# Optimization experiments

Measured on AMD Instinct MI355X. Metric: run time of the kernel, lower is better.

## Reference

```python
import jax, jax.numpy as jnp
import numpy as np

NQ = 11          # qubits per atom
NL = 3           # circuit layers (and message-passing layers)
S = 2 ** NQ      # statevector size
PAD = 100        # feature-map input width


def setup_inputs() -> dict:
    key = jax.random.key(0)
    ks = jax.random.split(key, 18)
    B, A, F, E = 8, 96, 64, 384
    return {
        "node_features": jax.random.normal(ks[0], (B, A, F), jnp.float32),
        "edge_indices": jax.random.randint(ks[1], (2, E), 0, A),
        # QuantumFeatureMap.feature_preprocessor: Linear(100,64) -> ReLU -> Linear(64,NQ) -> Tanh
        "W1": jax.random.normal(ks[2], (64, PAD), jnp.float32) * 0.1,
        "b1": jnp.zeros((64,), jnp.float32),
        "W2": jax.random.normal(ks[3], (NQ, 64), jnp.float32) * 0.1,
        "b2": jnp.zeros((NQ,), jnp.float32),
        # QuantumFeatureMap circuit params
        "rot": jax.random.normal(ks[4], (NL, NQ, 3), jnp.float32),
        "ent": jax.random.normal(ks[5], (NL, NQ - 1), jnp.float32),
        # one QuantumMessagePassing layer per NL, each with message_gates [NQ,3]
        "msg_gates": jax.random.normal(ks[6], (NL, NQ, 3), jnp.float32),
        # QuantumGlobalPooling
        "pool_w": jax.random.normal(ks[7], (NQ,), jnp.float32),
        # output MLP: Linear(2*NQ,256)->ReLU->Linear(256,128)->ReLU->Linear(128,64)
        "Wo1": jax.random.normal(ks[8], (256, 2 * NQ), jnp.float32) * 0.1,
        "bo1": jnp.zeros((256,), jnp.float32),
        "Wo2": jax.random.normal(ks[9], (128, 256), jnp.float32) * 0.05,
        "bo2": jnp.zeros((128,), jnp.float32),
        "Wo3": jax.random.normal(ks[10], (64, 128), jnp.float32) * 0.05,
        "bo3": jnp.zeros((64,), jnp.float32),
    }


def _apply_rotation(amps, M, q):
    """Apply per-batch 2x2 gate M [N,2,2] on qubit q of amps [N,S]."""
    N = amps.shape[0]
    lo = 1 << q
    hi = S // (2 * lo)
    a = amps.reshape(N, hi, 2, lo)  # bit q of state index is the middle axis
    return jnp.einsum('nij,nhjl->nhil', M, a).reshape(N, S)


def _forward(node_features, W1, b1, W2, b2, rot, ent, msg_gates, pool_w,
             Wo1, bo1, Wo2, bo2, Wo3, bo3):
    B, A, F = node_features.shape
    N = B * A
    # --- QuantumNodeEmbedding: pad atom features to 100, shared feature map ---
    x = node_features.reshape(N, F)
    x = jnp.pad(x, ((0, 0), (0, PAD - F)))
    h = jax.nn.relu(x @ W1.T + b1)
    f = jnp.tanh(h @ W2.T + b2)            # [N, NQ] per-qubit angles scaling
    amps = jnp.zeros((N, S), jnp.complex64).at[:, 0].set(1.0)
    states = jnp.arange(S)
    # --- QuantumFeatureMap circuit ---
    for l in range(NL):
        for q in range(NQ):
            rx = rot[l, q, 0] * f[:, q]
            ry = rot[l, q, 1] * f[:, q]
            rz = rot[l, q, 2] * f[:, q]
            cx, sx = jnp.cos(rx / 2), jnp.sin(rx / 2)
            cy, sy = jnp.cos(ry / 2), jnp.sin(ry / 2)
            cz, sz = jnp.cos(rz / 2), jnp.sin(rz / 2)
            # rotation matrix exactly as in the torch source
            M = jnp.stack([cx * cy * cz, -sx * sy * sz,
                           sx * sy * cz,  cx * cy * sz], -1)
            M = M.reshape(N, 2, 2).astype(jnp.complex64)
            amps = _apply_rotation(amps, M, q)
        for q in range(NQ - 1):
            # parameterized CNOT: for control-bit==1, mix state with target-flipped partner
            p = jax.nn.sigmoid(ent[l, q]).astype(jnp.complex64)
            ctrl = (states >> q) & 1
            partner = states ^ (1 << (q + 1))
            mixed = (1 - p) * amps + p * amps[:, partner]
            amps = jnp.where(ctrl[None, :] == 1, mixed, amps)
    # --- QuantumMessagePassing layers: diagonal phase exp(i*sum(theta_q over set bits)) ---
    bits = ((states[:, None] >> jnp.arange(NQ)[None, :]) & 1).astype(jnp.float32)  # [S,NQ]
    for l in range(NL):
        theta = msg_gates[l].sum(-1)                 # [NQ] rx+ry+rz per qubit
        phase = jnp.exp(1j * (bits @ theta))         # [S] complex64
        amps = amps * phase[None, :]
    # --- QuantumGlobalPooling ---
    amps_b = amps.reshape(B, A, S)
    w = jax.nn.sigmoid(pool_w[jnp.arange(A) % NQ]).astype(jnp.complex64)  # atom i -> w[i%NQ]
    pooled = jnp.einsum('a,bas->bs', w, amps_b)      # [B,S] complex
    norm = jnp.sqrt(jnp.sum(pooled.real ** 2 + pooled.imag ** 2, axis=1, keepdims=True))
    pooled = pooled / jnp.maximum(norm, 1e-12)
    rm = jnp.tile(pooled.real.mean(1, keepdims=True), (1, NQ))
    im = jnp.tile(pooled.imag.mean(1, keepdims=True), (1, NQ))
    rep = jnp.concatenate([rm, im], axis=1)          # [B, 2*NQ]
    # --- output network ---
    h1 = jax.nn.relu(rep @ Wo1.T + bo1)
    h2 = jax.nn.relu(h1 @ Wo2.T + bo2)
    return h2 @ Wo3.T + bo3                          # [B, 64]


def reference(node_features, edge_indices, W1, b1, W2, b2, rot, ent, msg_gates,
              pool_w, Wo1, bo1, Wo2, bo2, Wo3, bo3):
    # edge_indices is accepted by the torch module but does not enter the math
    del edge_indices
    return _forward(node_features, W1, b1, W2, b2, rot, ent, msg_gates, pool_w,
                    Wo1, bo1, Wo2, bo2, Wo3, bo3)
```

## Files before the change

kernel.cpp:

```cpp
#include <hip/hip_runtime.h>

#define NQ 11
#define NL 3
#define S  2048
#define NB 8
#define NA 96
#define NF 64
#define PADW 100
#define WPB 4
#define PPB (NA / WPB)

__device__ __forceinline__ float sigmoidf_(float x) { return 1.0f / (1.0f + expf(-x)); }

__global__ __launch_bounds__(256) void circuit_kernel(
    const float* __restrict__ nf,
    const float* __restrict__ W1,
    const float* __restrict__ b1,
    const float* __restrict__ W2,
    const float* __restrict__ b2,
    const float* __restrict__ rot,
    const float* __restrict__ ent,
    const float* __restrict__ pool_w,
    float* __restrict__ Rpart)
{
    __shared__ float W1s[64 * 65];
    __shared__ float xs[WPB][64];
    __shared__ float psum[WPB][S];

    const int tid   = threadIdx.x;
    const int lane  = tid & 63;
    const int wave  = tid >> 6;
    const int node0 = blockIdx.x * WPB;
    const int node  = node0 + wave;
    const int a     = node % NA;

    {
        const int r  = tid >> 2;
        const int c0 = (tid & 3) << 4;
        const float4* src = reinterpret_cast<const float4*>(W1 + r * PADW + c0);
        float* dst = &W1s[r * 65 + c0];
#pragma unroll
        for (int j = 0; j < 4; ++j) {
            const float4 vv = src[j];
            dst[4 * j + 0] = vv.x; dst[4 * j + 1] = vv.y;
            dst[4 * j + 2] = vv.z; dst[4 * j + 3] = vv.w;
        }
        xs[wave][lane] = nf[node0 * NF + tid];
    }
    __syncthreads();

    float h = b1[lane];
    {
        const float* wrow = &W1s[lane * 65];
        const float* xv   = xs[wave];
#pragma unroll
        for (int k = 0; k < 64; ++k) h = fmaf(wrow[k], xv[k], h);
    }
    h = fmaxf(h, 0.0f);

    float fscal = 0.0f;
#pragma unroll
    for (int q = 0; q < NQ; ++q) {
        float t = h * W2[q * 64 + lane];
#pragma unroll
        for (int off = 32; off >= 1; off >>= 1) t += __shfl_xor(t, off, 64);
        if (lane == q) fscal = tanhf(t + b2[q]);
    }

    const int qidx = lane < 11 ? lane : (lane < 22 ? lane - 11 : (lane < 33 ? lane - 22 : 0));
    const float fg = __shfl(fscal, qidx, 64);
    float m00 = 0.f, m01 = 0.f, m10 = 0.f, m11 = 0.f;
    if (lane < NL * NQ) {
        const float* r = rot + lane * 3;
        const float hx = 0.5f * r[0] * fg;
        const float hy = 0.5f * r[1] * fg;
        const float hz = 0.5f * r[2] * fg;
        const float cx = cosf(hx), sx = sinf(hx);
        const float cy = cosf(hy), sy = sinf(hy);
        const float cz = cosf(hz), sz = sinf(hz);
        m00 = cx * cy * cz; m01 = -sx * sy * sz;
        m10 = sx * sy * cz; m11 = cx * cy * sz;
    }
    float pent = 0.0f;
    if (lane < NL * (NQ - 1)) pent = sigmoidf_(ent[lane]);

    float v[32];
#pragma unroll
    for (int i = 0; i < 32; ++i) v[i] = 0.0f;
    if (lane == 0) v[0] = 1.0f;

    for (int l = 0; l < NL; ++l) {
#pragma unroll
        for (int q = 0; q < NQ; ++q) {
            const int g = l * NQ + q;
            const float g00 = __shfl(m00, g, 64);
            const float g01 = __shfl(m01, g, 64);
            const float g10 = __shfl(m10, g, 64);
            const float g11 = __shfl(m11, g, 64);
            if (q < 6) {
                const int   bit = (lane >> q) & 1;
                const float c0  = bit ? g10 : g01;
                const float c1  = bit ? g11 : g00;
#pragma unroll
                for (int i = 0; i < 32; ++i) {
                    const float pv = __shfl_xor(v[i], 1 << q, 64);
                    v[i] = fmaf(c0, pv, c1 * v[i]);
                }
            } else {
                const int rb = 1 << (q - 6);
#pragma unroll
                for (int j = 0; j < 16; ++j) {
                    const int i0 = ((j >> (q - 6)) << (q - 5)) | (j & (rb - 1));
                    const int i1 = i0 | rb;
                    const float a0 = v[i0], a1 = v[i1];
                    v[i0] = fmaf(g00, a0, g01 * a1);
                    v[i1] = fmaf(g10, a0, g11 * a1);
                }
            }
        }
#pragma unroll
        for (int q = 0; q < NQ - 1; ++q) {
            const float p = __shfl(pent, l * (NQ - 1) + q, 64);
            if (q < 5) {
                const float pact = p * (float)((lane >> q) & 1);
#pragma unroll
                for (int i = 0; i < 32; ++i) {
                    const float pv = __shfl_xor(v[i], 1 << (q + 1), 64);
                    v[i] = fmaf(pact, pv - v[i], v[i]);
                }
            } else if (q == 5) {
                const float pact = p * (float)((lane >> 5) & 1);
#pragma unroll
                for (int j = 0; j < 16; ++j) {
                    const int i0 = 2 * j, i1 = 2 * j + 1;
                    const float d = v[i1] - v[i0];
                    v[i0] = fmaf(pact, d, v[i0]);
                    v[i1] = fmaf(-pact, d, v[i1]);
                }
            } else {
                const int cb = q - 6;
#pragma unroll
                for (int j = 0; j < 8; ++j) {
                    const int i0 = ((j >> cb) << (cb + 2)) | (1 << cb) | (j & ((1 << cb) - 1));
                    const int i1 = i0 | (1 << (cb + 1));
                    const float d = v[i1] - v[i0];
                    v[i0] = fmaf(p, d, v[i0]);
                    v[i1] = fmaf(-p, d, v[i1]);
                }
            }
        }
    }

    const float w = sigmoidf_(pool_w[a % NQ]);
#pragma unroll
    for (int i = 0; i < 32; ++i) psum[wave][(i << 6) | lane] = w * v[i];
    __syncthreads();
    float* Rb = Rpart + blockIdx.x * S;
    for (int s = tid; s < S; s += 256)
        Rb[s] = psum[0][s] + psum[1][s] + psum[2][s] + psum[3][s];
}

__global__ __launch_bounds__(1024) void pool_mlp_kernel(
    const float* __restrict__ Rpart,
    const float* __restrict__ msg,
    const float* __restrict__ Wo1, const float* __restrict__ bo1,
    const float* __restrict__ Wo2, const float* __restrict__ bo2,
    const float* __restrict__ Wo3, const float* __restrict__ bo3,
    float* __restrict__ out)
{
    __shared__ float Theta[NQ];
    __shared__ float red[3][16];
    __shared__ float rm_sh, im_sh;
    __shared__ float h1[256];
    __shared__ float h2[128];

    const int b   = blockIdx.x;
    const int tid = threadIdx.x;

    if (tid < NQ) {
        float t = 0.0f;
        for (int l = 0; l < NL; ++l)
#pragma unroll
            for (int c = 0; c < 3; ++c) t += msg[(l * NQ + tid) * 3 + c];
        Theta[tid] = t;
    }
    __syncthreads();

    float psq = 0.0f, pc = 0.0f, ps = 0.0f;
    const float* Pb = Rpart + b * PPB * S;
    for (int s = tid; s < S; s += 1024) {
        float R = 0.0f;
#pragma unroll
        for (int j = 0; j < PPB; ++j) R += Pb[j * S + s];
        float phi = 0.0f;
#pragma unroll
        for (int q = 0; q < NQ; ++q)
            if ((s >> q) & 1) phi += Theta[q];
        psq += R * R;
        pc  += R * cosf(phi);
        ps  += R * sinf(phi);
    }
#pragma unroll
    for (int off = 32; off >= 1; off >>= 1) {
        psq += __shfl_xor(psq, off, 64);
        pc  += __shfl_xor(pc,  off, 64);
        ps  += __shfl_xor(ps,  off, 64);
    }
    const int lane = tid & 63, wave = tid >> 6;
    if (lane == 0) { red[0][wave] = psq; red[1][wave] = pc; red[2][wave] = ps; }
    __syncthreads();
    if (tid == 0) {
        float sq = 0.f, sc = 0.f, ss = 0.f;
#pragma unroll
        for (int wv = 0; wv < 16; ++wv) { sq += red[0][wv]; sc += red[1][wv]; ss += red[2][wv]; }
        const float norm = fmaxf(sqrtf(sq), 1e-12f);
        rm_sh = sc / (float)S / norm;
        im_sh = ss / (float)S / norm;
    }
    __syncthreads();
    const float rm = rm_sh, im = im_sh;

    if (tid < 256) {
        float s1 = 0.0f, s2 = 0.0f;
        const float* wrow = Wo1 + tid * (2 * NQ);
#pragma unroll
        for (int k = 0; k < NQ; ++k)       s1 += wrow[k];
#pragma unroll
        for (int k = NQ; k < 2 * NQ; ++k)  s2 += wrow[k];
        h1[tid] = fmaxf(rm * s1 + im * s2 + bo1[tid], 0.0f);
    }
    __syncthreads();
    if (tid < 128) {
        float acc = bo2[tid];
        const float* wrow = Wo2 + tid * 256;
        for (int k = 0; k < 256; ++k) acc += h1[k] * wrow[k];
        h2[tid] = fmaxf(acc, 0.0f);
    }
    __syncthreads();
    if (tid < 64) {
        float acc = bo3[tid];
        const float* wrow = Wo3 + tid * 128;
        for (int k = 0; k < 128; ++k) acc += h2[k] * wrow[k];
        out[b * 64 + tid] = acc;
    }
}

extern "C" void kernel_launch(void* const* d_in, const int* in_sizes, int n_in,
                              void* d_out, int out_size, void* d_ws, size_t ws_size,
                              hipStream_t stream) {
    const float* nf     = (const float*)d_in[0];
    const float* W1     = (const float*)d_in[2];
    const float* b1     = (const float*)d_in[3];
    const float* W2     = (const float*)d_in[4];
    const float* b2     = (const float*)d_in[5];
    const float* rot    = (const float*)d_in[6];
    const float* ent    = (const float*)d_in[7];
    const float* msg    = (const float*)d_in[8];
    const float* pool_w = (const float*)d_in[9];
    const float* Wo1    = (const float*)d_in[10];
    const float* bo1    = (const float*)d_in[11];
    const float* Wo2    = (const float*)d_in[12];
    const float* bo2    = (const float*)d_in[13];
    const float* Wo3    = (const float*)d_in[14];
    const float* bo3    = (const float*)d_in[15];

    float* Rpart = (float*)d_ws;

    circuit_kernel<<<dim3(NB * NA / WPB), dim3(256), 0, stream>>>(
        nf, W1, b1, W2, b2, rot, ent, pool_w, Rpart);

    pool_mlp_kernel<<<dim3(NB), dim3(1024), 0, stream>>>(
        Rpart, msg, Wo1, bo1, Wo2, bo2, Wo3, bo3, (float*)d_out);
}
```

Baseline: 123.0 us.

## Fuse circuit and pooling kernels with flag sync; use DPP/swizzle packed-pair gates

Merges the circuit and pooling/MLP kernels into one launch. The first block of each batch spins on per-block release flags, then reduces the partial statevectors and runs the MLP. This removes the second kernel launch and the dependency gap between them. The statevector is also stored as 16 packed float pairs, which turns qubit 6 into an in-register component swap. Cross-lane exchanges use DPP or ds_swizzle, and gate coefficients are broadcast with readlane instead of generic shuffles. Risks: the flags are never reset, so later calls can read stale flags and race on the partial sums. The spin-wait also depends on all blocks being co-resident.

```diff
diff --git a/kernel.cpp b/kernel.cpp
--- a/kernel.cpp
+++ b/kernel.cpp
@@ -9,10 +9,103 @@
 #define PADW 100
 #define WPB 4
 #define PPB (NA / WPB)
+#define NBLK (NB * NA / WPB)
+#define MAGIC 0x13572468u
+
+typedef float v2f __attribute__((ext_vector_type(2)));
 
 __device__ __forceinline__ float sigmoidf_(float x) { return 1.0f / (1.0f + expf(-x)); }
 
-__global__ __launch_bounds__(256) void circuit_kernel(
+__device__ __forceinline__ float rl_(float v, int srclane) {
+    return __builtin_bit_cast(float, __builtin_amdgcn_readlane(__builtin_bit_cast(int, v), srclane));
+}
+
+template<int M> __device__ __forceinline__ float sxf(float x) {
+    if constexpr (M == 1)
+        return __builtin_bit_cast(float, __builtin_amdgcn_mov_dpp(__builtin_bit_cast(int, x), 0xB1, 0xF, 0xF, true));
+    else if constexpr (M == 2)
+        return __builtin_bit_cast(float, __builtin_amdgcn_mov_dpp(__builtin_bit_cast(int, x), 0x4E, 0xF, 0xF, true));
+    else if constexpr (M == 8)
+        return __builtin_bit_cast(float, __builtin_amdgcn_mov_dpp(__builtin_bit_cast(int, x), 0x128, 0xF, 0xF, true));
+    else if constexpr (M == 4)
+        return __builtin_bit_cast(float, __builtin_amdgcn_ds_swizzle(__builtin_bit_cast(int, x), 0x101F));
+    else if constexpr (M == 16)
+        return __builtin_bit_cast(float, __builtin_amdgcn_ds_swizzle(__builtin_bit_cast(int, x), 0x401F));
+    else
+        return __shfl_xor(x, 32, 64);
+}
+template<int M> __device__ __forceinline__ v2f sxv(v2f w) {
+    v2f r; r.x = sxf<M>(w.x); r.y = sxf<M>(w.y); return r;
+}
+
+template<int Q> __device__ __forceinline__ void rot_lane(v2f* w, float g00, float g01,
+                                                         float g10, float g11, int lane) {
+    const int bit  = (lane >> Q) & 1;
+    const float c1 = bit ? g11 : g00;
+    const float c0 = bit ? g10 : g01;
+#pragma unroll
+    for (int j = 0; j < 16; ++j) {
+        v2f pw = sxv<(1 << Q)>(w[j]);
+        w[j] = c1 * w[j] + c0 * pw;
+    }
+}
+__device__ __forceinline__ void rot_comp(v2f* w, float g00, float g01, float g10, float g11) {
+    v2f ca; ca.x = g00; ca.y = g11;
+    v2f cb; cb.x = g01; cb.y = g10;
+#pragma unroll
+    for (int j = 0; j < 16; ++j) {
+        v2f sw; sw.x = w[j].y; sw.y = w[j].x;
+        w[j] = ca * w[j] + cb * sw;
+    }
+}
+template<int B> __device__ __forceinline__ void rot_reg(v2f* w, float g00, float g01,
+                                                        float g10, float g11) {
+#pragma unroll
+    for (int t = 0; t < 8; ++t) {
+        const int j0 = ((t >> B) << (B + 1)) | (t & ((1 << B) - 1));
+        const int j1 = j0 | (1 << B);
+        v2f a0 = w[j0], a1 = w[j1];
+        w[j0] = g00 * a0 + g01 * a1;
+        w[j1] = g10 * a0 + g11 * a1;
+    }
+}
+template<int Q> __device__ __forceinline__ void ent_lane(v2f* w, float p, int lane) {
+    const float pact = p * (float)((lane >> Q) & 1);
+#pragma unroll
+    for (int j = 0; j < 16; ++j) {
+        v2f pw = sxv<(1 << (Q + 1))>(w[j]);
+        w[j] = w[j] + pact * (pw - w[j]);
+    }
+}
+__device__ __forceinline__ void ent_5(v2f* w, float p, int lane) {
+    const float pact = p * (float)((lane >> 5) & 1);
+#pragma unroll
+    for (int j = 0; j < 16; ++j) {
+        v2f sw; sw.x = w[j].y; sw.y = w[j].x;
+        w[j] = w[j] + pact * (sw - w[j]);
+    }
+}
+__device__ __forceinline__ void ent_6(v2f* w, float p) {
+#pragma unroll
+    for (int t = 0; t < 8; ++t) {
+        const int j0 = 2 * t, j1 = 2 * t + 1;
+        const float d = w[j1].y - w[j0].y;
+        w[j0].y = fmaf(p, d, w[j0].y);
+        w[j1].y = fmaf(-p, d, w[j1].y);
+    }
+}
+template<int B> __device__ __forceinline__ void ent_reg(v2f* w, float p) {
+#pragma unroll
+    for (int t = 0; t < 4; ++t) {
+        const int j0 = ((t >> B) << (B + 2)) | (1 << B) | (t & ((1 << B) - 1));
+        const int j1 = j0 | (1 << (B + 1));
+        v2f d = w[j1] - w[j0];
+        w[j0] = w[j0] + p * d;
+        w[j1] = w[j1] - p * d;
+    }
+}
+
+__global__ __launch_bounds__(256) void fused_kernel(
     const float* __restrict__ nf,
     const float* __restrict__ W1,
     const float* __restrict__ b1,
@@ -20,19 +113,32 @@
     const float* __restrict__ b2,
     const float* __restrict__ rot,
     const float* __restrict__ ent,
+    const float* __restrict__ msg,
     const float* __restrict__ pool_w,
-    float* __restrict__ Rpart)
+    const float* __restrict__ Wo1, const float* __restrict__ bo1,
+    const float* __restrict__ Wo2, const float* __restrict__ bo2,
+    const float* __restrict__ Wo3, const float* __restrict__ bo3,
+    float* __restrict__ Rpart,
+    unsigned* __restrict__ flags,
+    float* __restrict__ out)
 {
     __shared__ float W1s[64 * 65];
     __shared__ float xs[WPB][64];
     __shared__ float psum[WPB][S];
-
-    const int tid   = threadIdx.x;
-    const int lane  = tid & 63;
-    const int wave  = tid >> 6;
-    const int node0 = blockIdx.x * WPB;
-    const int node  = node0 + wave;
-    const int a     = node % NA;
+    __shared__ float Theta[NQ];
+    __shared__ float red[3][WPB];
+    __shared__ float rm_sh, im_sh;
+    __shared__ float h1[256];
+    __shared__ float h2[128];
+
+    const int tid  = threadIdx.x;
+    const int lane = tid & 63;
+    const int wave = tid >> 6;
+    const int blk  = blockIdx.x;
+    const int bb   = blk / PPB;
+    const int pb   = blk % PPB;
+    const int node = blk * WPB + wave;
+    const int a    = node % NA;
 
     {
         const int r  = tid >> 2;
@@ -45,7 +151,7 @@
             dst[4 * j + 0] = vv.x; dst[4 * j + 1] = vv.y;
             dst[4 * j + 2] = vv.z; dst[4 * j + 3] = vv.w;
         }
-        xs[wave][lane] = nf[node0 * NF + tid];
+        xs[wave][lane] = nf[blk * WPB * NF + tid];
     }
     __syncthreads();
 
@@ -84,98 +190,53 @@
     float pent = 0.0f;
     if (lane < NL * (NQ - 1)) pent = sigmoidf_(ent[lane]);
 
-    float v[32];
-#pragma unroll
-    for (int i = 0; i < 32; ++i) v[i] = 0.0f;
-    if (lane == 0) v[0] = 1.0f;
+    v2f w[16];
+#pragma unroll
+    for (int j = 0; j < 16; ++j) { w[j].x = 0.0f; w[j].y = 0.0f; }
+    if (lane == 0) w[0].x = 1.0f;
+
+#define GC(G) const int gi = gb + (G); \
+    const float g00 = rl_(m00, gi), g01 = rl_(m01, gi), g10 = rl_(m10, gi), g11 = rl_(m11, gi)
+#define ROTL(Q) { GC(Q); rot_lane<Q>(w, g00, g01, g10, g11, lane); }
+#define ROTR(B) { GC((B) + 7); rot_reg<B>(w, g00, g01, g10, g11); }
+#define ENTL(Q) { const float p = rl_(pent, eb + (Q)); ent_lane<Q>(w, p, lane); }
 
     for (int l = 0; l < NL; ++l) {
-#pragma unroll
-        for (int q = 0; q < NQ; ++q) {
-            const int g = l * NQ + q;
-            const float g00 = __shfl(m00, g, 64);
-            const float g01 = __shfl(m01, g, 64);
-            const float g10 = __shfl(m10, g, 64);
-            const float g11 = __shfl(m11, g, 64);
-            if (q < 6) {
-                const int   bit = (lane >> q) & 1;
-                const float c0  = bit ? g10 : g01;
-                const float c1  = bit ? g11 : g00;
-#pragma unroll
-                for (int i = 0; i < 32; ++i) {
-                    const float pv = __shfl_xor(v[i], 1 << q, 64);
-                    v[i] = fmaf(c0, pv, c1 * v[i]);
-                }
-            } else {
-                const int rb = 1 << (q - 6);
-#pragma unroll
-                for (int j = 0; j < 16; ++j) {
-                    const int i0 = ((j >> (q - 6)) << (q - 5)) | (j & (rb - 1));
-                    const int i1 = i0 | rb;
-                    const float a0 = v[i0], a1 = v[i1];
-                    v[i0] = fmaf(g00, a0, g01 * a1);
-                    v[i1] = fmaf(g10, a0, g11 * a1);
-                }
-            }
+        const int gb = l * NQ;
+        const int eb = l * (NQ - 1);
+        ROTL(0) ROTL(1) ROTL(2) ROTL(3) ROTL(4) ROTL(5)
+        { GC(6); rot_comp(w, g00, g01, g10, g11); }
+        ROTR(0) ROTR(1) ROTR(2) ROTR(3)
+        ENTL(0) ENTL(1) ENTL(2) ENTL(3) ENTL(4)
+        { const float p = rl_(pent, eb + 5); ent_5(w, p, lane); }
+        { const float p = rl_(pent, eb + 6); ent_6(w, p); }
+        { const float p = rl_(pent, eb + 7); ent_reg<0>(w, p); }
+        { const float p = rl_(pent, eb + 8); ent_reg<1>(w, p); }
+        { const float p = rl_(pent, eb + 9); ent_reg<2>(w, p); }
+    }
+
+    const float wgt = sigmoidf_(pool_w[a % NQ]);
+#pragma unroll
+    for (int j = 0; j < 16; ++j) {
+        psum[wave][((2 * j + 0) << 6) | lane] = wgt * w[j].x;
+        psum[wave][((2 * j + 1) << 6) | lane] = wgt * w[j].y;
+    }
+    __syncthreads();
+    {
+        float* Rb = Rpart + (size_t)blk * S;
+        for (int s = tid; s < S; s += 256) {
+            const float sum = psum[0][s] + psum[1][s] + psum[2][s] + psum[3][s];
+            Rb[s] = sum;
+            psum[0][s] = sum;
         }
-#pragma unroll
-        for (int q = 0; q < NQ - 1; ++q) {
-            const float p = __shfl(pent, l * (NQ - 1) + q, 64);
-            if (q < 5) {
-                const float pact = p * (float)((lane >> q) & 1);
-#pragma unroll
-                for (int i = 0; i < 32; ++i) {
-                    const float pv = __shfl_xor(v[i], 1 << (q + 1), 64);
-                    v[i] = fmaf(pact, pv - v[i], v[i]);
-                }
-            } else if (q == 5) {
-                const float pact = p * (float)((lane >> 5) & 1);
-#pragma unroll
-                for (int j = 0; j < 16; ++j) {
-                    const int i0 = 2 * j, i1 = 2 * j + 1;
-                    const float d = v[i1] - v[i0];
-                    v[i0] = fmaf(pact, d, v[i0]);
-                    v[i1] = fmaf(-pact, d, v[i1]);
-                }
-            } else {
-                const int cb = q - 6;
-#pragma unroll
-                for (int j = 0; j < 8; ++j) {
-                    const int i0 = ((j >> cb) << (cb + 2)) | (1 << cb) | (j & ((1 << cb) - 1));
-                    const int i1 = i0 | (1 << (cb + 1));
-                    const float d = v[i1] - v[i0];
-                    v[i0] = fmaf(p, d, v[i0]);
-                    v[i1] = fmaf(-p, d, v[i1]);
-                }
-            }
-        }
-    }
-
-    const float w = sigmoidf_(pool_w[a % NQ]);
-#pragma unroll
-    for (int i = 0; i < 32; ++i) psum[wave][(i << 6) | lane] = w * v[i];
-    __syncthreads();
-    float* Rb = Rpart + blockIdx.x * S;
-    for (int s = tid; s < S; s += 256)
-        Rb[s] = psum[0][s] + psum[1][s] + psum[2][s] + psum[3][s];
-}
-
-__global__ __launch_bounds__(1024) void pool_mlp_kernel(
-    const float* __restrict__ Rpart,
-    const float* __restrict__ msg,
-    const float* __restrict__ Wo1, const float* __restrict__ bo1,
-    const float* __restrict__ Wo2, const float* __restrict__ bo2,
-    const float* __restrict__ Wo3, const float* __restrict__ bo3,
-    float* __restrict__ out)
-{
-    __shared__ float Theta[NQ];
-    __shared__ float red[3][16];
-    __shared__ float rm_sh, im_sh;
-    __shared__ float h1[256];
-    __shared__ float h2[128];
-
-    const int b   = blockIdx.x;
-    const int tid = threadIdx.x;
+    }
+    __syncthreads();
+    if (tid == 0) {
+        __threadfence();
+        __hip_atomic_store(&flags[blk], MAGIC, __ATOMIC_RELEASE, __HIP_MEMORY_SCOPE_AGENT);
+    }
+
+    if (pb != 0) return;
 
     if (tid < NQ) {
         float t = 0.0f;
@@ -184,21 +245,29 @@
             for (int c = 0; c < 3; ++c) t += msg[(l * NQ + tid) * 3 + c];
         Theta[tid] = t;
     }
-    __syncthreads();
+    if (tid < PPB - 1) {
+        const unsigned* fp = flags + bb * PPB + 1 + tid;
+        while (__hip_atomic_load(fp, __ATOMIC_RELAXED, __HIP_MEMORY_SCOPE_AGENT) != MAGIC)
+            __builtin_amdgcn_s_sleep(2);
+    }
+    __syncthreads();
+    __threadfence();
 
     float psq = 0.0f, pc = 0.0f, ps = 0.0f;
-    const float* Pb = Rpart + b * PPB * S;
-    for (int s = tid; s < S; s += 1024) {
-        float R = 0.0f;
-#pragma unroll
-        for (int j = 0; j < PPB; ++j) R += Pb[j * S + s];
-        float phi = 0.0f;
-#pragma unroll
-        for (int q = 0; q < NQ; ++q)
-            if ((s >> q) & 1) phi += Theta[q];
-        psq += R * R;
-        pc  += R * cosf(phi);
-        ps  += R * sinf(phi);
+    {
+        const float* Pb = Rpart + (size_t)bb * PPB * S;
+        for (int s = tid; s < S; s += 256) {
+            float R = psum[0][s];
+#pragma unroll
+            for (int j = 1; j < PPB; ++j) R += Pb[(size_t)j * S + s];
+            float phi = 0.0f;
+#pragma unroll
+            for (int q = 0; q < NQ; ++q)
+                if ((s >> q) & 1) phi += Theta[q];
+            psq += R * R;
+            pc  += R * cosf(phi);
+            ps  += R * sinf(phi);
+        }
     }
 #pragma unroll
     for (int off = 32; off >= 1; off >>= 1) {
@@ -206,13 +275,12 @@
         pc  += __shfl_xor(pc,  off, 64);
         ps  += __shfl_xor(ps,  off, 64);
     }
-    const int lane = tid & 63, wave = tid >> 6;
     if (lane == 0) { red[0][wave] = psq; red[1][wave] = pc; red[2][wave] = ps; }
     __syncthreads();
     if (tid == 0) {
         float sq = 0.f, sc = 0.f, ss = 0.f;
 #pragma unroll
-        for (int wv = 0; wv < 16; ++wv) { sq += red[0][wv]; sc += red[1][wv]; ss += red[2][wv]; }
+        for (int wv = 0; wv < WPB; ++wv) { sq += red[0][wv]; sc += red[1][wv]; ss += red[2][wv]; }
         const float norm = fmaxf(sqrtf(sq), 1e-12f);
         rm_sh = sc / (float)S / norm;
         im_sh = ss / (float)S / norm;
@@ -220,7 +288,7 @@
     __syncthreads();
     const float rm = rm_sh, im = im_sh;
 
-    if (tid < 256) {
+    {
         float s1 = 0.0f, s2 = 0.0f;
         const float* wrow = Wo1 + tid * (2 * NQ);
 #pragma unroll
@@ -241,7 +309,7 @@
         float acc = bo3[tid];
         const float* wrow = Wo3 + tid * 128;
         for (int k = 0; k < 128; ++k) acc += h2[k] * wrow[k];
-        out[b * 64 + tid] = acc;
+        out[bb * 64 + tid] = acc;
     }
 }
 
@@ -264,11 +332,10 @@
     const float* Wo3    = (const float*)d_in[14];
     const float* bo3    = (const float*)d_in[15];
 
-    float* Rpart = (float*)d_ws;
-
-    circuit_kernel<<<dim3(NB * NA / WPB), dim3(256), 0, stream>>>(
-        nf, W1, b1, W2, b2, rot, ent, pool_w, Rpart);
-
-    pool_mlp_kernel<<<dim3(NB), dim3(1024), 0, stream>>>(
-        Rpart, msg, Wo1, bo1, Wo2, bo2, Wo3, bo3, (float*)d_out);
-}
+    float*    Rpart = (float*)d_ws;
+    unsigned* flags = (unsigned*)(Rpart + NBLK * S);
+
+    fused_kernel<<<dim3(NBLK), dim3(256), 0, stream>>>(
+        nf, W1, b1, W2, b2, rot, ent, msg, pool_w,
+        Wo1, bo1, Wo2, bo2, Wo3, bo3, Rpart, flags, (float*)d_out);
+}
```

New measurement: 126.0 us. 2.4% more time.
